# Optimization experiments

Hardware: AMD Instinct MI355X
Metric: run time of the kernel (lower is better)

## Reference

```python
import jax, jax.numpy as jnp
import numpy as np

B, S, HID, HEADS = 1, 512, 1024, 16
HD = HID // HEADS          # 64
LN_EPS = 1e-5
EPS = 1e-8


def setup_inputs() -> dict:
    key = jax.random.key(0)
    ks = jax.random.split(key, 10)
    def w(k, fan_in, shape):
        return (jax.random.normal(k, shape, jnp.float32) / np.sqrt(fan_in)).astype(jnp.float32)
    return {
        "x": jax.random.normal(ks[0], (B, S, HID), jnp.float32),
        "attention_mask": jnp.ones((B, S), jnp.int32),
        "Wq": w(ks[1], HID, (HID, HID)), "bq": jnp.zeros((HID,), jnp.float32),
        "Wk": w(ks[2], HID, (HID, HID)), "bk": jnp.zeros((HID,), jnp.float32),
        "Wv": w(ks[3], HID, (HID, HID)), "bv": jnp.zeros((HID,), jnp.float32),
        "Wo": w(ks[4], HID, (HID, HID)), "bo": jnp.zeros((HID,), jnp.float32),
        "temperature": jnp.ones((1,), jnp.float32),
        "ln_gamma": jnp.ones((HID,), jnp.float32),
        "ln_beta": jnp.zeros((HID,), jnp.float32),
    }


def _forward(x, attention_mask, Wq, bq, Wk, bk, Wv, bv, Wo, bo, temperature, ln_gamma, ln_beta):
    b, s, hid = x.shape
    residual = x
    def proj(W, bias):  # [b,s,hid] -> [b,H,s,hd]
        return (x @ W + bias).reshape(b, s, HEADS, HD).transpose(0, 2, 1, 3)
    Q, K, V = proj(Wq, bq), proj(Wk, bk), proj(Wv, bv)
    # FFT over head_dim -> F = HD//2+1 frequency bins
    Qf = jnp.fft.rfft(Q, axis=-1)
    Kf = jnp.fft.rfft(K, axis=-1)
    Qa, Ka = jnp.abs(Qf), jnp.abs(Kf)
    Qp, Kp = jnp.angle(Qf), jnp.angle(Kf)
    # broadcast to [b,H,Sq,Sk,F]; eps lives inside sqrt (faithful, non-factorized)
    amp_w = jnp.sqrt(Qa[:, :, :, None, :] * Ka[:, :, None, :, :] + EPS)
    phase_align = jnp.cos(Qp[:, :, :, None, :] - Kp[:, :, None, :, :])
    scores = jnp.sum(phase_align * amp_w, axis=-1) * temperature  # [b,H,Sq,Sk]
    mask = attention_mask[:, None, None, :]  # [b,1,1,Sk]
    scores = jnp.where(mask == 0, jnp.float32(-1e9), scores)
    attn = jax.nn.softmax(scores, axis=-1)   # dropout omitted (eval mode)
    out = jnp.einsum('bhqk,bhkd->bhqd', attn, V)
    out = out.transpose(0, 2, 1, 3).reshape(b, s, hid)
    out = out @ Wo + bo
    y = residual + out
    mu = jnp.mean(y, axis=-1, keepdims=True)
    var = jnp.var(y, axis=-1, keepdims=True)
    return (y - mu) / jnp.sqrt(var + LN_EPS) * ln_gamma + ln_beta


def reference(x, attention_mask, Wq, bq, Wk, bk, Wv, bv, Wo, bo, temperature, ln_gamma, ln_beta):
    return _forward(x, attention_mask, Wq, bq, Wk, bk, Wv, bv, Wo, bo,
                    temperature, ln_gamma, ln_beta)
```

## Files before the change

### kernel.cpp

```cpp
#include <hip/hip_runtime.h>
#include <hip/hip_bf16.h>
#include <math.h>

constexpr int SEQ   = 512;
constexpr int HIDC  = 1024;
constexpr int NH    = 16;
constexpr int HDIM  = 64;
constexpr int NFREQ = 33;
constexpr int NFP   = 128;

typedef unsigned short u16;
typedef __bf16 bf16x8 __attribute__((ext_vector_type(8)));
typedef float  f32x4  __attribute__((ext_vector_type(4)));
typedef unsigned short u16x8 __attribute__((ext_vector_type(8)));

typedef __attribute__((address_space(3))) void       as3_void;
typedef __attribute__((address_space(1))) const void as1_void;

__device__ __forceinline__ void gload16(const u16* g, u16* l) {
    __builtin_amdgcn_global_load_lds((as1_void*)g, (as3_void*)l, 16, 0, 0);
}

__device__ __forceinline__ float ldin(const void* p, int i, int f32) {
    if (f32) return ((const float*)p)[i];
    return __bfloat162float(((const __hip_bfloat16*)p)[i]);
}

__device__ __forceinline__ u16 f2b(float f) {
    unsigned int u = __builtin_bit_cast(unsigned int, f);
    u += 0x7fffu + ((u >> 16) & 1u);
    return (u16)(u >> 16);
}
__device__ __forceinline__ float b2f(u16 b) {
    return __builtin_bit_cast(float, (unsigned int)b << 16);
}
__device__ __forceinline__ void split2(float f, u16& hi, u16& lo) {
    hi = f2b(f);
    lo = f2b(f - b2f(hi));
}

__device__ __forceinline__ int sniffF(const u16* wq) {
    const int lane = threadIdx.x & 63;
    const ushort4 a = *(const ushort4*)(wq + lane * 8);
    const ushort4 b = *(const ushort4*)(wq + lane * 8 + 4);
    int bad = 0;
    {
        const u16 vs[8] = {a.x, a.y, a.z, a.w, b.x, b.y, b.z, b.w};
        #pragma unroll
        for (int j = 0; j < 8; ++j)
            if (((vs[j] >> 7) & 0xFF) >= 134) bad++;
    }
    #pragma unroll
    for (int off = 32; off > 0; off >>= 1) bad += __shfl_xor(bad, off, 64);
    return (bad > 32) ? 1 : 0;
}

__global__ __launch_bounds__(256) void prep_kernel(
    const void* __restrict__ W0, const void* __restrict__ W1,
    const void* __restrict__ W2, const void* __restrict__ W3,
    u16* __restrict__ H0, u16* __restrict__ L0,
    u16* __restrict__ H1, u16* __restrict__ L1,
    u16* __restrict__ H2, u16* __restrict__ L2,
    u16* __restrict__ H3, u16* __restrict__ L3,
    const void* __restrict__ xsrc, u16* __restrict__ xhi, u16* __restrict__ xlo)
{
    const int F  = sniffF((const u16*)W0);
    const int mz = blockIdx.z;

    if (mz == 4) {
        const int blk = blockIdx.y * 16 + blockIdx.x;
        const int i0  = blk * 2048 + threadIdx.x * 8;
        #pragma unroll
        for (int g = 0; g < 2; ++g) {
            const int i = i0 + g * 4;
            float v[4];
            if (F) {
                const float4 f = *(const float4*)((const float*)xsrc + i);
                v[0] = f.x; v[1] = f.y; v[2] = f.z; v[3] = f.w;
            } else {
                #pragma unroll
                for (int j = 0; j < 4; ++j) v[j] = ldin(xsrc, i + j, 0);
            }
            ushort4 oh, ol;
            u16 h, l;
            split2(v[0], h, l); oh.x = h; ol.x = l;
            split2(v[1], h, l); oh.y = h; ol.y = l;
            split2(v[2], h, l); oh.z = h; ol.z = l;
            split2(v[3], h, l); oh.w = h; ol.w = l;
            *(ushort4*)&xhi[i] = oh;
            *(ushort4*)&xlo[i] = ol;
        }
        return;
    }

    __shared__ float t[64][65];
    const void* W = (mz == 0) ? W0 : (mz == 1) ? W1 : (mz == 2) ? W2 : W3;
    u16* H = (mz == 0) ? H0 : (mz == 1) ? H1 : (mz == 2) ? H2 : H3;
    u16* L = (mz == 0) ? L0 : (mz == 1) ? L1 : (mz == 2) ? L2 : L3;
    const int n0 = blockIdx.x * 64, k0 = blockIdx.y * 64;
    const int tid = threadIdx.x;

    #pragma unroll
    for (int i = 0; i < 4; ++i) {
        const int item = i * 256 + tid;
        const int r = item >> 4, c4 = (item & 15) * 4;
        if (F) {
            const float4 v = *(const float4*)((const float*)W + (k0 + r) * HIDC + n0 + c4);
            t[r][c4 + 0] = v.x; t[r][c4 + 1] = v.y; t[r][c4 + 2] = v.z; t[r][c4 + 3] = v.w;
        } else {
            #pragma unroll
            for (int j = 0; j < 4; ++j)
                t[r][c4 + j] = ldin(W, (k0 + r) * HIDC + n0 + c4 + j, 0);
        }
    }
    __syncthreads();
    #pragma unroll
    for (int i = 0; i < 4; ++i) {
        const int item = i * 256 + tid;
        const int r = item >> 4, c4 = (item & 15) * 4;
        ushort4 oh, ol;
        u16 h, l;
        split2(t[c4 + 0][r], h, l); oh.x = h; ol.x = l;
        split2(t[c4 + 1][r], h, l); oh.y = h; ol.y = l;
        split2(t[c4 + 2][r], h, l); oh.z = h; ol.z = l;
        split2(t[c4 + 3][r], h, l); oh.w = h; ol.w = l;
        *(ushort4*)&H[(n0 + r) * HIDC + k0 + c4] = oh;
        *(ushort4*)&L[(n0 + r) * HIDC + k0 + c4] = ol;
    }
}

template <int MODE, int MT>
__global__ __launch_bounds__(256) void mfma3_gemm_kernel(
    const u16* __restrict__ Ahi, const u16* __restrict__ Alo,
    const u16* __restrict__ B0h, const u16* __restrict__ B0l,
    const u16* __restrict__ B1h, const u16* __restrict__ B1l,
    const u16* __restrict__ B2h, const u16* __restrict__ B2l,
    const void* __restrict__ b0, const void* __restrict__ b1, const void* __restrict__ b2,
    const void* __restrict__ xres,
    u16* __restrict__ Qh, u16* __restrict__ Ql,
    u16* __restrict__ Kh, u16* __restrict__ Kl,
    u16* __restrict__ Vth, u16* __restrict__ Vtl,
    float* __restrict__ Yout,
    const void* __restrict__ wq_sniff)
{
    constexpr int NMI = MT / 16;
    constexpr int NAC = MT / 32;
    constexpr int ACH = MT * 64;
    constexpr int BUF = 2 * ACH + 16384;
    __shared__ __align__(16) u16 smem[2 * BUF];

    const int F    = sniffF((const u16*)wq_sniff);
    const int tid  = threadIdx.x;
    const int lane = tid & 63, wv = tid >> 6;
    const int m0 = blockIdx.y * MT;
    const int n0 = blockIdx.x * 128;

    const u16 *Bh, *Bl; const void* bias; int col0, mat = 0;
    if (MODE == 0) {
        mat  = n0 >> 10;
        col0 = n0 & 1023;
        Bh   = (mat == 0) ? B0h : (mat == 1) ? B1h : B2h;
        Bl   = (mat == 0) ? B0l : (mat == 1) ? B1l : B2l;
        bias = (mat == 0) ? b0  : (mat == 1) ? b1  : b2;
    } else {
        col0 = n0; Bh = B0h; Bl = B0l; bias = b0;
    }

    const int rsub = lane >> 3;
    const int gsw  = ((lane & 7) ^ rsub) * 8;
    const u16* pAh[2]; const u16* pAl[2];
    const u16* pBh[4]; const u16* pBl[4];
    int dA[2], dB[4];
    #pragma unroll
    for (int j = 0; j < NAC; ++j) {
        const int c = wv * NAC + j;
        pAh[j] = Ahi + (m0 + c * 8 + rsub) * HIDC + gsw;
        pAl[j] = Alo + (m0 + c * 8 + rsub) * HIDC + gsw;
        dA[j]  = c * 512;
    }
    #pragma unroll
    for (int j = 0; j < 4; ++j) {
        const int c = wv * 4 + j;
        pBh[j] = Bh + (col0 + c * 8 + rsub) * HIDC + gsw;
        pBl[j] = Bl + (col0 + c * 8 + rsub) * HIDC + gsw;
        dB[j]  = c * 512;
    }

    int g16[2];
    #pragma unroll
    for (int kc = 0; kc < 2; ++kc) g16[kc] = (((kc * 4) + (lane >> 4)) ^ (lane & 7)) * 8;
    int afo[4], bfo[2];
    #pragma unroll
    for (int mi = 0; mi < NMI; ++mi) afo[mi] = (mi * 16 + (lane & 15)) * 64;
    #pragma unroll
    for (int ni = 0; ni < 2; ++ni) bfo[ni] = (wv * 32 + ni * 16 + (lane & 15)) * 64;

    f32x4 acc[NMI][2];
    #pragma unroll
    for (int mi = 0; mi < NMI; ++mi)
        #pragma unroll
        for (int ni = 0; ni < 2; ++ni) acc[mi][ni] = f32x4{0.f, 0.f, 0.f, 0.f};

    #pragma unroll
    for (int j = 0; j < NAC; ++j) {
        gload16(pAh[j], smem + dA[j]);
        gload16(pAl[j], smem + ACH + dA[j]);
    }
    #pragma unroll
    for (int j = 0; j < 4; ++j) {
        gload16(pBh[j], smem + 2 * ACH + dB[j]);
        gload16(pBl[j], smem + 2 * ACH + 8192 + dB[j]);
    }
    __syncthreads();

    for (int t = 0; t < 16; ++t) {
        const int bo = (t & 1) * BUF;
        if (t < 15) {
            const int bn = BUF - bo;
            const int k  = (t + 1) * 64;
            #pragma unroll
            for (int j = 0; j < NAC; ++j) {
                gload16(pAh[j] + k, smem + bn + dA[j]);
                gload16(pAl[j] + k, smem + bn + ACH + dA[j]);
            }
            #pragma unroll
            for (int j = 0; j < 4; ++j) {
                gload16(pBh[j] + k, smem + bn + 2 * ACH + dB[j]);
                gload16(pBl[j] + k, smem + bn + 2 * ACH + 8192 + dB[j]);
            }
        }
        #pragma unroll
        for (int kc = 0; kc < 2; ++kc) {
            bf16x8 ah[NMI], al[NMI], bh2[2], bl2[2];
            #pragma unroll
            for (int mi = 0; mi < NMI; ++mi) {
                ah[mi] = *(const bf16x8*)(smem + bo +       afo[mi] + g16[kc]);
                al[mi] = *(const bf16x8*)(smem + bo + ACH + afo[mi] + g16[kc]);
            }
            #pragma unroll
            for (int ni = 0; ni < 2; ++ni) {
                bh2[ni] = *(const bf16x8*)(smem + bo + 2 * ACH +        bfo[ni] + g16[kc]);
                bl2[ni] = *(const bf16x8*)(smem + bo + 2 * ACH + 8192 + bfo[ni] + g16[kc]);
            }
            #pragma unroll
            for (int mi = 0; mi < NMI; ++mi)
                #pragma unroll
                for (int ni = 0; ni < 2; ++ni) {
                    acc[mi][ni] = __builtin_amdgcn_mfma_f32_16x16x32_bf16(
                        ah[mi], bh2[ni], acc[mi][ni], 0, 0, 0);
                    acc[mi][ni] = __builtin_amdgcn_mfma_f32_16x16x32_bf16(
                        ah[mi], bl2[ni], acc[mi][ni], 0, 0, 0);
                    acc[mi][ni] = __builtin_amdgcn_mfma_f32_16x16x32_bf16(
                        al[mi], bh2[ni], acc[mi][ni], 0, 0, 0);
                }
        }
        __syncthreads();
    }

    const int hi4 = (lane >> 4) * 4;
    #pragma unroll
    for (int ni = 0; ni < 2; ++ni) {
        const int col = col0 + wv * 32 + ni * 16 + (lane & 15);
        const float bval = ldin(bias, col, F);
        #pragma unroll
        for (int mi = 0; mi < NMI; ++mi) {
            const int row0 = m0 + mi * 16 + hi4;
            if (MODE == 1) {
                #pragma unroll
                for (int r = 0; r < 4; ++r) {
                    const int row = row0 + r;
                    Yout[row * HIDC + col] =
                        acc[mi][ni][r] + bval + ldin(xres, row * HIDC + col, F);
                }
            } else if (mat == 2) {
                ushort4 oh, ol;
                u16 h_, l_;
                split2(acc[mi][ni][0] + bval, h_, l_); oh.x = h_; ol.x = l_;
                split2(acc[mi][ni][1] + bval, h_, l_); oh.y = h_; ol.y = l_;
                split2(acc[mi][ni][2] + bval, h_, l_); oh.z = h_; ol.z = l_;
                split2(acc[mi][ni][3] + bval, h_, l_); oh.w = h_; ol.w = l_;
                *(ushort4*)&Vth[col * SEQ + row0] = oh;
                *(ushort4*)&Vtl[col * SEQ + row0] = ol;
            } else {
                u16* Oh = (mat == 0) ? Qh : Kh;
                u16* Ol = (mat == 0) ? Ql : Kl;
                #pragma unroll
                for (int r = 0; r < 4; ++r) {
                    u16 h_, l_;
                    split2(acc[mi][ni][r] + bval, h_, l_);
                    Oh[(row0 + r) * HIDC + col] = h_;
                    Ol[(row0 + r) * HIDC + col] = l_;
                }
            }
        }
    }
}

__global__ __launch_bounds__(256) void dft_kernel(
    const u16* __restrict__ Qmh, const u16* __restrict__ Qml,
    const u16* __restrict__ Kmh, const u16* __restrict__ Kml,
    u16* __restrict__ Qsh, u16* __restrict__ Qsl,
    u16* __restrict__ Ksh, u16* __restrict__ Ksl)
{
    __shared__ __align__(16) u16 smem[16384];
    __shared__ float tcos[64], tsin[64];

    const int tid  = threadIdx.x;
    const int lane = tid & 63, wv = tid >> 6;
    const int hi = lane >> 4, q15 = lane & 15, l7 = lane & 7;
    const int m0  = blockIdx.x * 64;
    const int sel = blockIdx.y;
    const u16* Ah_g = sel ? Kmh : Qmh;
    const u16* Al_g = sel ? Kml : Qml;
    u16* Oh = sel ? Ksh : Qsh;
    u16* Ol = sel ? Ksl : Qsl;

    const int rsub = lane >> 3;
    const int gsw  = ((lane & 7) ^ rsub) * 8;
    #pragma unroll
    for (int j = 0; j < 2; ++j) {
        const int c = wv * 2 + j;
        gload16(Ah_g + (m0 + c * 8 + rsub) * 64 + gsw, smem + c * 512);
        gload16(Al_g + (m0 + c * 8 + rsub) * 64 + gsw, smem + 4096 + c * 512);
    }
    if (tid < 64) {
        float sv, cv;
        sincosf((float)tid * (6.283185307179586f / 64.0f), &sv, &cv);
        tcos[tid] = cv; tsin[tid] = sv;
    }
    __syncthreads();

    bf16x8 Dh[2][2], Dl[2][2];
    #pragma unroll
    for (int ni = 0; ni < 2; ++ni) {
        const int c = wv * 32 + ni * 16 + q15;
        #pragma unroll
        for (int kc = 0; kc < 2; ++kc) {
            u16x8 bh_, bl_;
            #pragma unroll
            for (int e = 0; e < 8; ++e) {
                const int k = (kc * 4 + hi) * 8 + e;
                float dv;
                if (c < 33)      dv = tcos[(c * k) & 63];
                else if (c < 66) dv = -tsin[((c - 33) * k) & 63];
                else             dv = 0.0f;
                u16 h_, l_;
                split2(dv, h_, l_);
                bh_[e] = h_; bl_[e] = l_;
            }
            Dh[ni][kc] = __builtin_bit_cast(bf16x8, bh_);
            Dl[ni][kc] = __builtin_bit_cast(bf16x8, bl_);
        }
    }

    f32x4 acc[4][2];
    #pragma unroll
    for (int mi = 0; mi < 4; ++mi)
        #pragma unroll
        for (int ni = 0; ni < 2; ++ni) acc[mi][ni] = f32x4{0.f, 0.f, 0.f, 0.f};

    #pragma unroll
    for (int kc = 0; kc < 2; ++kc) {
        const int g = (((kc * 4) + hi) ^ l7) * 8;
        bf16x8 ah[4], al[4];
        #pragma unroll
        for (int mi = 0; mi < 4; ++mi) {
            ah[mi] = *(const bf16x8*)(smem +        (mi * 16 + q15) * 64 + g);
            al[mi] = *(const bf16x8*)(smem + 4096 + (mi * 16 + q15) * 64 + g);
        }
        #pragma unroll
        for (int mi = 0; mi < 4; ++mi)
            #pragma unroll
            for (int ni = 0; ni < 2; ++ni) {
                acc[mi][ni] = __builtin_amdgcn_mfma_f32_16x16x32_bf16(
                    ah[mi], Dh[ni][kc], acc[mi][ni], 0, 0, 0);
                acc[mi][ni] = __builtin_amdgcn_mfma_f32_16x16x32_bf16(
                    ah[mi], Dl[ni][kc], acc[mi][ni], 0, 0, 0);
                acc[mi][ni] = __builtin_amdgcn_mfma_f32_16x16x32_bf16(
                    al[mi], Dh[ni][kc], acc[mi][ni], 0, 0, 0);
            }
    }
    __syncthreads();

    float* Cl = (float*)smem;
    #pragma unroll
    for (int mi = 0; mi < 4; ++mi)
        #pragma unroll
        for (int ni = 0; ni < 2; ++ni)
            #pragma unroll
            for (int r = 0; r < 4; ++r)
                Cl[(mi * 16 + hi * 4 + r) * 128 + wv * 32 + ni * 16 + q15] = acc[mi][ni][r];
    __syncthreads();

    const int row = tid >> 2, tf = tid & 3;
    const int g   = m0 + row;
    const int ss  = g >> 4, hh = g & 15;
    u16 vh[32], vl[32];
    #pragma unroll
    for (int j = 0; j < 32; ++j) {
        const int f = tf * 32 + j;
        float val = 0.0f;
        if (f < 66) {
            const int fb = (f < 33) ? f : (f - 33);
            const float re = Cl[row * 128 + fb];
            const float im = Cl[row * 128 + 33 + fb];
            const float a  = sqrtf(re * re + im * im);
            const float sc = (a > 0.0f) ? rsqrtf(a) : 0.0f;
            val = ((f < 33) ? re : im) * sc;
        }
        split2(val, vh[j], vl[j]);
    }
    const int obase = (hh * SEQ + ss) * NFP + tf * 32;
    #pragma unroll
    for (int j4 = 0; j4 < 8; ++j4) {
        ushort4 oh, ol;
        oh.x = vh[j4 * 4 + 0]; oh.y = vh[j4 * 4 + 1]; oh.z = vh[j4 * 4 + 2]; oh.w = vh[j4 * 4 + 3];
        ol.x = vl[j4 * 4 + 0]; ol.y = vl[j4 * 4 + 1]; ol.z = vl[j4 * 4 + 2]; ol.w = vl[j4 * 4 + 3];
        *(ushort4*)&Oh[obase + j4 * 4] = oh;
        *(ushort4*)&Ol[obase + j4 * 4] = ol;
    }
}

__global__ __launch_bounds__(128) void attn_mfma_kernel(
    const u16* __restrict__ Qsh, const u16* __restrict__ Qsl,
    const u16* __restrict__ Ksh, const u16* __restrict__ Ksl,
    const u16* __restrict__ VTh, const u16* __restrict__ VTl,
    const int* __restrict__ mask, const void* __restrict__ temp_p,
    u16* __restrict__ chi, u16* __restrict__ clo,
    const void* __restrict__ wq_sniff)
{
    __shared__ __align__(16) u16 smem[32768];
    __shared__ int   mask_lds[512];
    __shared__ float mpart[2][16], lpart[2][16], l_final[16];

    const int F    = sniffF((const u16*)wq_sniff);
    const int tid  = threadIdx.x;
    const int lane = tid & 63, w = tid >> 6;
    const int hi = lane >> 4, q15 = lane & 15, l7 = lane & 7;
    const int h  = blockIdx.y, q0 = blockIdx.x * 16;
    const int k0 = w * 256;
    const int WB = w * 16384;
    const float temp = ldin(temp_p, 0, F);

    *(int4*)&mask_lds[tid * 4] = *(const int4*)&mask[tid * 4];

    bf16x8 qfh[3], qfl[3];
    {
        const int qrow = (h * SEQ + q0 + q15) * NFP;
        #pragma unroll
        for (int kc = 0; kc < 3; ++kc) {
            qfh[kc] = *(const bf16x8*)(Qsh + qrow + kc * 32 + hi * 8);
            qfl[kc] = *(const bf16x8*)(Qsl + qrow + kc * 32 + hi * 8);
        }
    }

    const int rc4 = lane >> 4;

    auto stageK = [&](int kt, int b) {
        const int base = WB + b * 8192;
        #pragma unroll
        for (int j = 0; j < 8; ++j) {
            const int row = j * 4 + rc4;
            const int gs  = (q15 ^ (row & 7)) * 8;
            const int so  = (h * SEQ + k0 + kt * 32 + row) * NFP + gs;
            gload16(Ksh + so, smem + base + j * 512);
            gload16(Ksl + so, smem + base + 4096 + j * 512);
        }
    };
    auto stageV = [&](int c, int b) {
        const int base = WB + b * 4096;
        #pragma unroll
        for (int j = 0; j < 4; ++j) {
            const int d  = j * 16 + (lane >> 2);
            const int gs = ((lane & 3) ^ (d & 3)) * 8;
            const int so = (h * HDIM + d) * SEQ + k0 + c * 32 + gs;
            gload16(VTh + so, smem + base + j * 512);
            gload16(VTl + so, smem + base + 2048 + j * 512);
        }
    };

    f32x4 sT[16];
    #pragma unroll
    for (int t = 0; t < 16; ++t) sT[t] = f32x4{0.f, 0.f, 0.f, 0.f};

    stageK(0, 0);
    #pragma unroll
    for (int kt = 0; kt < 8; ++kt) {
        if (kt < 7) {
            stageK(kt + 1, (kt + 1) & 1);
            asm volatile("s_waitcnt vmcnt(16)" ::: "memory");
        } else {
            asm volatile("s_waitcnt vmcnt(0)" ::: "memory");
        }
        __builtin_amdgcn_sched_barrier(0);
        const int base = WB + (kt & 1) * 8192;
        #pragma unroll
        for (int tt = 0; tt < 2; ++tt) {
            #pragma unroll
            for (int kc = 0; kc < 3; ++kc) {
                const int ro = (tt * 16 + q15) * 128 + (((kc * 4 + hi) ^ l7) * 8);
                const bf16x8 ah = *(const bf16x8*)(smem + base + ro);
                const bf16x8 al = *(const bf16x8*)(smem + base + 4096 + ro);
                sT[kt * 2 + tt] = __builtin_amdgcn_mfma_f32_16x16x32_bf16(ah, qfh[kc], sT[kt * 2 + tt], 0, 0, 0);
                sT[kt * 2 + tt] = __builtin_amdgcn_mfma_f32_16x16x32_bf16(ah, qfl[kc], sT[kt * 2 + tt], 0, 0, 0);
                sT[kt * 2 + tt] = __builtin_amdgcn_mfma_f32_16x16x32_bf16(al, qfh[kc], sT[kt * 2 + tt], 0, 0, 0);
            }
        }
    }

    __builtin_amdgcn_sched_barrier(0);
    stageV(0, 0);

    float m = -1e30f;
    #pragma unroll
    for (int t = 0; t < 16; ++t) {
        const int4 mv = *(const int4*)&mask_lds[k0 + t * 16 + hi * 4];
        float s;
        s = (mv.x == 0) ? -1e9f : sT[t][0] * temp; sT[t][0] = s; m = fmaxf(m, s);
        s = (mv.y == 0) ? -1e9f : sT[t][1] * temp; sT[t][1] = s; m = fmaxf(m, s);
        s = (mv.z == 0) ? -1e9f : sT[t][2] * temp; sT[t][2] = s; m = fmaxf(m, s);
        s = (mv.w == 0) ? -1e9f : sT[t][3] * temp; sT[t][3] = s; m = fmaxf(m, s);
    }
    m = fmaxf(m, __shfl_xor(m, 16, 64));
    m = fmaxf(m, __shfl_xor(m, 32, 64));
    if (lane < 16) mpart[w][q15] = m;
    __syncthreads();
    const float gm = fmaxf(mpart[0][q15], mpart[1][q15]);
    float sum = 0.0f;
    #pragma unroll
    for (int t = 0; t < 16; ++t) {
        #pragma unroll
        for (int r = 0; r < 4; ++r) {
            const float p = __expf(sT[t][r] - gm);
            sT[t][r] = p;
            sum += p;
        }
    }
    sum += __shfl_xor(sum, 16, 64);
    sum += __shfl_xor(sum, 32, 64);
    if (lane < 16) lpart[w][q15] = sum;
    __syncthreads();
    if (tid < 16) l_final[tid] = lpart[0][tid] + lpart[1][tid];

    const int PH = WB + 8192, PL = PH + 640;
    f32x4 acc[4];
    #pragma unroll
    for (int dt = 0; dt < 4; ++dt) acc[dt] = f32x4{0.f, 0.f, 0.f, 0.f};

    #pragma unroll
    for (int c = 0; c < 8; ++c) {
        if (c < 7) {
            stageV(c + 1, (c + 1) & 1);
            asm volatile("s_waitcnt vmcnt(8)" ::: "memory");
        } else {
            asm volatile("s_waitcnt vmcnt(0)" ::: "memory");
        }
        __builtin_amdgcn_sched_barrier(0);
        #pragma unroll
        for (int tt = 0; tt < 2; ++tt) {
            const int t = c * 2 + tt;
            ushort4 ph, pl;
            u16 hh, ll;
            split2(sT[t][0], hh, ll); ph.x = hh; pl.x = ll;
            split2(sT[t][1], hh, ll); ph.y = hh; pl.y = ll;
            split2(sT[t][2], hh, ll); ph.z = hh; pl.z = ll;
            split2(sT[t][3], hh, ll); ph.w = hh; pl.w = ll;
            const int g  = tt * 2 + (hi >> 1);
            const int po = q15 * 40 + ((g ^ (q15 & 3)) * 8) + (hi & 1) * 4;
            *(ushort4*)(smem + PH + po) = ph;
            *(ushort4*)(smem + PL + po) = pl;
        }
        const int vb  = WB + (c & 1) * 4096;
        const int pro = q15 * 40 + ((hi ^ (q15 & 3)) * 8);
        const bf16x8 pfh = *(const bf16x8*)(smem + PH + pro);
        const bf16x8 pfl = *(const bf16x8*)(smem + PL + pro);
        #pragma unroll
        for (int dt = 0; dt < 4; ++dt) {
            const int vo = (dt * 16 + q15) * 32 + ((hi ^ (q15 & 3)) * 8);
            const bf16x8 vfh = *(const bf16x8*)(smem + vb + vo);
            const bf16x8 vfl = *(const bf16x8*)(smem + vb + 2048 + vo);
            acc[dt] = __builtin_amdgcn_mfma_f32_16x16x32_bf16(pfh, vfh, acc[dt], 0, 0, 0);
            acc[dt] = __builtin_amdgcn_mfma_f32_16x16x32_bf16(pfl, vfh, acc[dt], 0, 0, 0);
            acc[dt] = __builtin_amdgcn_mfma_f32_16x16x32_bf16(pfh, vfl, acc[dt], 0, 0, 0);
        }
    }

    float* pacc = (float*)(smem + WB + 12288);
    #pragma unroll
    for (int dt = 0; dt < 4; ++dt)
        *(f32x4*)&pacc[(dt * 64 + lane) * 4] = acc[dt];
    __syncthreads();
    const float* pa0 = (const float*)(smem + 12288);
    const float* pa1 = (const float*)(smem + 16384 + 12288);
    #pragma unroll
    for (int dd = 0; dd < 2; ++dd) {
        const int dt = w * 2 + dd;
        #pragma unroll
        for (int r = 0; r < 4; ++r) {
            const int idx = (dt * 64 + lane) * 4 + r;
            const float v = (pa0[idx] + pa1[idx]) / l_final[hi * 4 + r];
            u16 hh, ll;
            split2(v, hh, ll);
            const int row = q0 + hi * 4 + r;
            const int col = h * HDIM + dt * 16 + q15;
            chi[row * HIDC + col] = hh;
            clo[row * HIDC + col] = ll;
        }
    }
}

__global__ __launch_bounds__(256) void ln_kernel(
    const float* __restrict__ Y, const void* __restrict__ gamma,
    const void* __restrict__ beta, void* __restrict__ out,
    const void* __restrict__ wq_sniff)
{
    const int F = sniffF((const u16*)wq_sniff);
    const int row = blockIdx.x, tid = threadIdx.x;
    float v[4];
    float s = 0.0f, s2 = 0.0f;
    #pragma unroll
    for (int j = 0; j < 4; ++j) {
        v[j] = Y[row * HIDC + tid + j * 256];
        s += v[j]; s2 += v[j] * v[j];
    }
    #pragma unroll
    for (int off = 32; off > 0; off >>= 1) {
        s  += __shfl_xor(s, off, 64);
        s2 += __shfl_xor(s2, off, 64);
    }
    __shared__ float wred[4][2];
    const int w = tid >> 6;
    if ((tid & 63) == 0) { wred[w][0] = s; wred[w][1] = s2; }
    __syncthreads();
    s  = wred[0][0] + wred[1][0] + wred[2][0] + wred[3][0];
    s2 = wred[0][1] + wred[1][1] + wred[2][1] + wred[3][1];
    const float mu   = s / (float)HIDC;
    const float var  = s2 / (float)HIDC - mu * mu;
    const float rstd = rsqrtf(var + 1e-5f);
    #pragma unroll
    for (int j = 0; j < 4; ++j) {
        const int c = tid + j * 256;
        const float g = ldin(gamma, c, F), b = ldin(beta, c, F);
        const float r = (v[j] - mu) * rstd * g + b;
        if (F) ((float*)out)[row * HIDC + c] = r;
        else   ((__hip_bfloat16*)out)[row * HIDC + c] = __float2bfloat16(r);
    }
}

extern "C" void kernel_launch(void* const* d_in, const int* in_sizes, int n_in,
                              void* d_out, int out_size, void* d_ws, size_t ws_size,
                              hipStream_t stream) {
    const void* x    = d_in[0];
    const int*  mask = (const int*)d_in[1];
    const void* Wq   = d_in[2];
    const void* bq   = d_in[3];
    const void* Wk   = d_in[4];
    const void* bk   = d_in[5];
    const void* Wv   = d_in[6];
    const void* bv   = d_in[7];
    const void* Wo   = d_in[8];
    const void* bo   = d_in[9];
    const void* temp = d_in[10];
    const void* gam  = d_in[11];
    const void* bet  = d_in[12];

    float* Y    = (float*)d_ws;
    u16*   xhi  = (u16*)(Y + SEQ * HIDC);
    u16*   xlo  = xhi + SEQ * HIDC;
    u16*   chi  = xlo + SEQ * HIDC;
    u16*   clo  = chi + SEQ * HIDC;
    u16*   Qmh  = clo + SEQ * HIDC;
    u16*   Qml  = Qmh + SEQ * HIDC;
    u16*   Kmh  = Qml + SEQ * HIDC;
    u16*   Kml  = Kmh + SEQ * HIDC;
    u16*   VTh  = Kml + SEQ * HIDC;
    u16*   VTl  = VTh + NH * HDIM * SEQ;
    u16*   Wqh  = VTl + NH * HDIM * SEQ;
    u16*   Wql  = Wqh + HIDC * HIDC;
    u16*   Wkh  = Wql + HIDC * HIDC;
    u16*   Wkl  = Wkh + HIDC * HIDC;
    u16*   Wvh  = Wkl + HIDC * HIDC;
    u16*   Wvl  = Wvh + HIDC * HIDC;
    u16*   Woh  = Wvl + HIDC * HIDC;
    u16*   Wol  = Woh + HIDC * HIDC;
    u16*   Qsh  = Wol + HIDC * HIDC;
    u16*   Qsl  = Qsh + NH * SEQ * NFP;
    u16*   Ksh  = Qsl + NH * SEQ * NFP;
    u16*   Ksl  = Ksh + NH * SEQ * NFP;

    prep_kernel<<<dim3(16, 16, 5), 256, 0, stream>>>(
        Wq, Wk, Wv, Wo, Wqh, Wql, Wkh, Wkl, Wvh, Wvl, Woh, Wol,
        x, xhi, xlo);

    mfma3_gemm_kernel<0, 64><<<dim3(24, 8), 256, 0, stream>>>(
        xhi, xlo, Wqh, Wql, Wkh, Wkl, Wvh, Wvl,
        bq, bk, bv, nullptr,
        Qmh, Qml, Kmh, Kml, VTh, VTl, nullptr, Wq);

    dft_kernel<<<dim3(128, 2), 256, 0, stream>>>(
        Qmh, Qml, Kmh, Kml, Qsh, Qsl, Ksh, Ksl);

    attn_mfma_kernel<<<dim3(SEQ / 16, NH), 128, 0, stream>>>(
        Qsh, Qsl, Ksh, Ksl, VTh, VTl, mask, temp, chi, clo, Wq);

    mfma3_gemm_kernel<1, 32><<<dim3(8, 16), 256, 0, stream>>>(
        chi, clo, Woh, Wol, nullptr, nullptr, nullptr, nullptr,
        bo, nullptr, nullptr, x,
        nullptr, nullptr, nullptr, nullptr, nullptr, nullptr, Y, Wq);

    ln_kernel<<<SEQ, 256, 0, stream>>>(Y, gam, bet, d_out, Wq);
}
```

Measured before the change: 161.6 us.

## Fuse head-dim DFT and amplitude normalization into QKV projection GEMM epilogue

The separate DFT kernel is removed. The QKV GEMM epilogue now stages each 64x128 output tile (two heads) in shared memory, runs the 64-point DFT with split-bf16 MFMAs per head, applies the amplitude normalization, and writes the spectral Q/K buffers directly. This drops one kernel launch and the round trip of the intermediate Q/K projections through global memory. In exchange the Q and K GEMM blocks carry a longer serial epilogue with extra syncs and LDS traffic, which may lengthen the critical path of that kernel.

```diff
diff --git a/kernel.cpp b/kernel.cpp
--- a/kernel.cpp
+++ b/kernel.cpp
@@ -137,8 +137,8 @@
     const u16* __restrict__ B2h, const u16* __restrict__ B2l,
     const void* __restrict__ b0, const void* __restrict__ b1, const void* __restrict__ b2,
     const void* __restrict__ xres,
-    u16* __restrict__ Qh, u16* __restrict__ Ql,
-    u16* __restrict__ Kh, u16* __restrict__ Kl,
+    u16* __restrict__ Qsh, u16* __restrict__ Qsl,
+    u16* __restrict__ Ksh, u16* __restrict__ Ksl,
     u16* __restrict__ Vth, u16* __restrict__ Vtl,
     float* __restrict__ Yout,
     const void* __restrict__ wq_sniff)
@@ -148,10 +148,13 @@
     constexpr int ACH = MT * 64;
     constexpr int BUF = 2 * ACH + 16384;
     __shared__ __align__(16) u16 smem[2 * BUF];
+    __shared__ float tcs[64], tsn[64];
 
     const int F    = sniffF((const u16*)wq_sniff);
     const int tid  = threadIdx.x;
     const int lane = tid & 63, wv = tid >> 6;
+    const int q15 = lane & 15, hi = lane >> 4, l7 = lane & 7;
+    const int hi4 = hi * 4;
     const int m0 = blockIdx.y * MT;
     const int n0 = blockIdx.x * 128;
 
@@ -188,12 +191,12 @@
 
     int g16[2];
     #pragma unroll
-    for (int kc = 0; kc < 2; ++kc) g16[kc] = (((kc * 4) + (lane >> 4)) ^ (lane & 7)) * 8;
+    for (int kc = 0; kc < 2; ++kc) g16[kc] = (((kc * 4) + hi) ^ l7) * 8;
     int afo[4], bfo[2];
     #pragma unroll
-    for (int mi = 0; mi < NMI; ++mi) afo[mi] = (mi * 16 + (lane & 15)) * 64;
-    #pragma unroll
-    for (int ni = 0; ni < 2; ++ni) bfo[ni] = (wv * 32 + ni * 16 + (lane & 15)) * 64;
+    for (int mi = 0; mi < NMI; ++mi) afo[mi] = (mi * 16 + q15) * 64;
+    #pragma unroll
+    for (int ni = 0; ni < 2; ++ni) bfo[ni] = (wv * 32 + ni * 16 + q15) * 64;
 
     f32x4 acc[NMI][2];
     #pragma unroll
@@ -257,22 +260,30 @@
         __syncthreads();
     }
 
-    const int hi4 = (lane >> 4) * 4;
-    #pragma unroll
-    for (int ni = 0; ni < 2; ++ni) {
-        const int col = col0 + wv * 32 + ni * 16 + (lane & 15);
-        const float bval = ldin(bias, col, F);
-        #pragma unroll
-        for (int mi = 0; mi < NMI; ++mi) {
-            const int row0 = m0 + mi * 16 + hi4;
-            if (MODE == 1) {
+    if (MODE == 1) {
+        #pragma unroll
+        for (int ni = 0; ni < 2; ++ni) {
+            const int col = col0 + wv * 32 + ni * 16 + q15;
+            const float bval = ldin(bias, col, F);
+            #pragma unroll
+            for (int mi = 0; mi < NMI; ++mi) {
+                const int row0 = m0 + mi * 16 + hi4;
                 #pragma unroll
                 for (int r = 0; r < 4; ++r) {
                     const int row = row0 + r;
                     Yout[row * HIDC + col] =
                         acc[mi][ni][r] + bval + ldin(xres, row * HIDC + col, F);
                 }
-            } else if (mat == 2) {
+            }
+        }
+    } else if (mat == 2) {
+        #pragma unroll
+        for (int ni = 0; ni < 2; ++ni) {
+            const int col = col0 + wv * 32 + ni * 16 + q15;
+            const float bval = ldin(bias, col, F);
+            #pragma unroll
+            for (int mi = 0; mi < NMI; ++mi) {
+                const int row0 = m0 + mi * 16 + hi4;
                 ushort4 oh, ol;
                 u16 h_, l_;
                 split2(acc[mi][ni][0] + bval, h_, l_); oh.x = h_; ol.x = l_;
@@ -281,143 +292,138 @@
                 split2(acc[mi][ni][3] + bval, h_, l_); oh.w = h_; ol.w = l_;
                 *(ushort4*)&Vth[col * SEQ + row0] = oh;
                 *(ushort4*)&Vtl[col * SEQ + row0] = ol;
-            } else {
-                u16* Oh = (mat == 0) ? Qh : Kh;
-                u16* Ol = (mat == 0) ? Ql : Kl;
-                #pragma unroll
-                for (int r = 0; r < 4; ++r) {
+            }
+        }
+    } else {
+        float* Cf = (float*)smem;
+        #pragma unroll
+        for (int ni = 0; ni < 2; ++ni) {
+            const int c = wv * 32 + ni * 16 + q15;
+            const float bval = ldin(bias, col0 + c, F);
+            #pragma unroll
+            for (int mi = 0; mi < NMI; ++mi)
+                #pragma unroll
+                for (int r = 0; r < 4; ++r)
+                    Cf[(mi * 16 + hi4 + r) * 128 + c] = acc[mi][ni][r] + bval;
+        }
+        if (tid < 64) {
+            float sv, cv;
+            sincosf((float)tid * (6.283185307179586f / 64.0f), &sv, &cv);
+            tcs[tid] = cv; tsn[tid] = sv;
+        }
+        __syncthreads();
+
+        bf16x8 Dh[2][2], Dl[2][2];
+        #pragma unroll
+        for (int ni = 0; ni < 2; ++ni) {
+            const int c = wv * 32 + ni * 16 + q15;
+            #pragma unroll
+            for (int kc = 0; kc < 2; ++kc) {
+                u16x8 bh_, bl_;
+                #pragma unroll
+                for (int e = 0; e < 8; ++e) {
+                    const int k = (kc * 4 + hi) * 8 + e;
+                    float dv;
+                    if (c < 33)      dv = tcs[(c * k) & 63];
+                    else if (c < 66) dv = -tsn[((c - 33) * k) & 63];
+                    else             dv = 0.0f;
                     u16 h_, l_;
-                    split2(acc[mi][ni][r] + bval, h_, l_);
-                    Oh[(row0 + r) * HIDC + col] = h_;
-                    Ol[(row0 + r) * HIDC + col] = l_;
+                    split2(dv, h_, l_);
+                    bh_[e] = h_; bl_[e] = l_;
                 }
-            }
-        }
-    }
-}
-
-__global__ __launch_bounds__(256) void dft_kernel(
-    const u16* __restrict__ Qmh, const u16* __restrict__ Qml,
-    const u16* __restrict__ Kmh, const u16* __restrict__ Kml,
-    u16* __restrict__ Qsh, u16* __restrict__ Qsl,
-    u16* __restrict__ Ksh, u16* __restrict__ Ksl)
-{
-    __shared__ __align__(16) u16 smem[16384];
-    __shared__ float tcos[64], tsin[64];
-
-    const int tid  = threadIdx.x;
-    const int lane = tid & 63, wv = tid >> 6;
-    const int hi = lane >> 4, q15 = lane & 15, l7 = lane & 7;
-    const int m0  = blockIdx.x * 64;
-    const int sel = blockIdx.y;
-    const u16* Ah_g = sel ? Kmh : Qmh;
-    const u16* Al_g = sel ? Kml : Qml;
-    u16* Oh = sel ? Ksh : Qsh;
-    u16* Ol = sel ? Ksl : Qsl;
-
-    const int rsub = lane >> 3;
-    const int gsw  = ((lane & 7) ^ rsub) * 8;
-    #pragma unroll
-    for (int j = 0; j < 2; ++j) {
-        const int c = wv * 2 + j;
-        gload16(Ah_g + (m0 + c * 8 + rsub) * 64 + gsw, smem + c * 512);
-        gload16(Al_g + (m0 + c * 8 + rsub) * 64 + gsw, smem + 4096 + c * 512);
-    }
-    if (tid < 64) {
-        float sv, cv;
-        sincosf((float)tid * (6.283185307179586f / 64.0f), &sv, &cv);
-        tcos[tid] = cv; tsin[tid] = sv;
-    }
-    __syncthreads();
-
-    bf16x8 Dh[2][2], Dl[2][2];
-    #pragma unroll
-    for (int ni = 0; ni < 2; ++ni) {
-        const int c = wv * 32 + ni * 16 + q15;
-        #pragma unroll
-        for (int kc = 0; kc < 2; ++kc) {
-            u16x8 bh_, bl_;
-            #pragma unroll
-            for (int e = 0; e < 8; ++e) {
-                const int k = (kc * 4 + hi) * 8 + e;
-                float dv;
-                if (c < 33)      dv = tcos[(c * k) & 63];
-                else if (c < 66) dv = -tsin[((c - 33) * k) & 63];
-                else             dv = 0.0f;
-                u16 h_, l_;
-                split2(dv, h_, l_);
-                bh_[e] = h_; bl_[e] = l_;
-            }
-            Dh[ni][kc] = __builtin_bit_cast(bf16x8, bh_);
-            Dl[ni][kc] = __builtin_bit_cast(bf16x8, bl_);
-        }
-    }
-
-    f32x4 acc[4][2];
-    #pragma unroll
-    for (int mi = 0; mi < 4; ++mi)
-        #pragma unroll
-        for (int ni = 0; ni < 2; ++ni) acc[mi][ni] = f32x4{0.f, 0.f, 0.f, 0.f};
-
-    #pragma unroll
-    for (int kc = 0; kc < 2; ++kc) {
-        const int g = (((kc * 4) + hi) ^ l7) * 8;
-        bf16x8 ah[4], al[4];
-        #pragma unroll
-        for (int mi = 0; mi < 4; ++mi) {
-            ah[mi] = *(const bf16x8*)(smem +        (mi * 16 + q15) * 64 + g);
-            al[mi] = *(const bf16x8*)(smem + 4096 + (mi * 16 + q15) * 64 + g);
-        }
-        #pragma unroll
-        for (int mi = 0; mi < 4; ++mi)
-            #pragma unroll
-            for (int ni = 0; ni < 2; ++ni) {
-                acc[mi][ni] = __builtin_amdgcn_mfma_f32_16x16x32_bf16(
-                    ah[mi], Dh[ni][kc], acc[mi][ni], 0, 0, 0);
-                acc[mi][ni] = __builtin_amdgcn_mfma_f32_16x16x32_bf16(
-                    ah[mi], Dl[ni][kc], acc[mi][ni], 0, 0, 0);
-                acc[mi][ni] = __builtin_amdgcn_mfma_f32_16x16x32_bf16(
-                    al[mi], Dh[ni][kc], acc[mi][ni], 0, 0, 0);
-            }
-    }
-    __syncthreads();
-
-    float* Cl = (float*)smem;
-    #pragma unroll
-    for (int mi = 0; mi < 4; ++mi)
-        #pragma unroll
-        for (int ni = 0; ni < 2; ++ni)
-            #pragma unroll
-            for (int r = 0; r < 4; ++r)
-                Cl[(mi * 16 + hi * 4 + r) * 128 + wv * 32 + ni * 16 + q15] = acc[mi][ni][r];
-    __syncthreads();
-
-    const int row = tid >> 2, tf = tid & 3;
-    const int g   = m0 + row;
-    const int ss  = g >> 4, hh = g & 15;
-    u16 vh[32], vl[32];
-    #pragma unroll
-    for (int j = 0; j < 32; ++j) {
-        const int f = tf * 32 + j;
-        float val = 0.0f;
-        if (f < 66) {
-            const int fb = (f < 33) ? f : (f - 33);
-            const float re = Cl[row * 128 + fb];
-            const float im = Cl[row * 128 + 33 + fb];
-            const float a  = sqrtf(re * re + im * im);
-            const float sc = (a > 0.0f) ? rsqrtf(a) : 0.0f;
-            val = ((f < 33) ? re : im) * sc;
-        }
-        split2(val, vh[j], vl[j]);
-    }
-    const int obase = (hh * SEQ + ss) * NFP + tf * 32;
-    #pragma unroll
-    for (int j4 = 0; j4 < 8; ++j4) {
-        ushort4 oh, ol;
-        oh.x = vh[j4 * 4 + 0]; oh.y = vh[j4 * 4 + 1]; oh.z = vh[j4 * 4 + 2]; oh.w = vh[j4 * 4 + 3];
-        ol.x = vl[j4 * 4 + 0]; ol.y = vl[j4 * 4 + 1]; ol.z = vl[j4 * 4 + 2]; ol.w = vl[j4 * 4 + 3];
-        *(ushort4*)&Oh[obase + j4 * 4] = oh;
-        *(ushort4*)&Ol[obase + j4 * 4] = ol;
+                Dh[ni][kc] = __builtin_bit_cast(bf16x8, bh_);
+                Dl[ni][kc] = __builtin_bit_cast(bf16x8, bl_);
+            }
+        }
+
+        u16* AH = smem + 16384;
+        u16* AL = smem + 20480;
+        float* C2 = (float*)(smem + 24576);
+        u16* Oh = (mat == 0) ? Qsh : Ksh;
+        u16* Ol = (mat == 0) ? Qsl : Ksl;
+
+        #pragma unroll
+        for (int head = 0; head < 2; ++head) {
+            const int hh = (col0 >> 6) + head;
+            {
+                const int row = tid >> 2;
+                const int d0  = (tid & 3) * 16;
+                const int rx  = row & 7;
+                #pragma unroll
+                for (int d = d0; d < d0 + 16; ++d) {
+                    const int src = (((d >> 3) ^ rx) * 8) + (d & 7);
+                    u16 h_, l_;
+                    split2(Cf[row * 128 + head * 64 + src], h_, l_);
+                    AH[row * 64 + d] = h_;
+                    AL[row * 64 + d] = l_;
+                }
+            }
+            __syncthreads();
+            f32x4 a2[4][2];
+            #pragma unroll
+            for (int mi = 0; mi < 4; ++mi)
+                #pragma unroll
+                for (int ni = 0; ni < 2; ++ni) a2[mi][ni] = f32x4{0.f, 0.f, 0.f, 0.f};
+            #pragma unroll
+            for (int kc = 0; kc < 2; ++kc) {
+                const int g = g16[kc];
+                bf16x8 ah2[4], al2[4];
+                #pragma unroll
+                for (int mi = 0; mi < 4; ++mi) {
+                    ah2[mi] = *(const bf16x8*)(AH + (mi * 16 + q15) * 64 + g);
+                    al2[mi] = *(const bf16x8*)(AL + (mi * 16 + q15) * 64 + g);
+                }
+                #pragma unroll
+                for (int mi = 0; mi < 4; ++mi)
+                    #pragma unroll
+                    for (int ni = 0; ni < 2; ++ni) {
+                        a2[mi][ni] = __builtin_amdgcn_mfma_f32_16x16x32_bf16(
+                            ah2[mi], Dh[ni][kc], a2[mi][ni], 0, 0, 0);
+                        a2[mi][ni] = __builtin_amdgcn_mfma_f32_16x16x32_bf16(
+                            ah2[mi], Dl[ni][kc], a2[mi][ni], 0, 0, 0);
+                        a2[mi][ni] = __builtin_amdgcn_mfma_f32_16x16x32_bf16(
+                            al2[mi], Dh[ni][kc], a2[mi][ni], 0, 0, 0);
+                    }
+            }
+            __syncthreads();
+            #pragma unroll
+            for (int mi = 0; mi < 4; ++mi)
+                #pragma unroll
+                for (int ni = 0; ni < 2; ++ni)
+                    #pragma unroll
+                    for (int r = 0; r < 4; ++r)
+                        C2[(mi * 16 + hi4 + r) * 128 + wv * 32 + ni * 16 + q15] = a2[mi][ni][r];
+            __syncthreads();
+            {
+                const int row = tid >> 2, tf = tid & 3;
+                u16 vh[32], vl[32];
+                #pragma unroll
+                for (int j = 0; j < 32; ++j) {
+                    const int f = tf * 32 + j;
+                    float val = 0.0f;
+                    if (f < 66) {
+                        const int fb = (f < 33) ? f : (f - 33);
+                        const float re = C2[row * 128 + fb];
+                        const float im = C2[row * 128 + 33 + fb];
+                        const float a  = sqrtf(re * re + im * im);
+                        const float sc = (a > 0.0f) ? rsqrtf(a) : 0.0f;
+                        val = ((f < 33) ? re : im) * sc;
+                    }
+                    split2(val, vh[j], vl[j]);
+                }
+                const int obase = (hh * SEQ + m0 + row) * NFP + tf * 32;
+                #pragma unroll
+                for (int j4 = 0; j4 < 8; ++j4) {
+                    ushort4 oh, ol;
+                    oh.x = vh[j4 * 4 + 0]; oh.y = vh[j4 * 4 + 1];
+                    oh.z = vh[j4 * 4 + 2]; oh.w = vh[j4 * 4 + 3];
+                    ol.x = vl[j4 * 4 + 0]; ol.y = vl[j4 * 4 + 1];
+                    ol.z = vl[j4 * 4 + 2]; ol.w = vl[j4 * 4 + 3];
+                    *(ushort4*)&Oh[obase + j4 * 4] = oh;
+                    *(ushort4*)&Ol[obase + j4 * 4] = ol;
+                }
+            }
+        }
     }
 }
 
@@ -669,11 +675,7 @@
     u16*   xlo  = xhi + SEQ * HIDC;
     u16*   chi  = xlo + SEQ * HIDC;
     u16*   clo  = chi + SEQ * HIDC;
-    u16*   Qmh  = clo + SEQ * HIDC;
-    u16*   Qml  = Qmh + SEQ * HIDC;
-    u16*   Kmh  = Qml + SEQ * HIDC;
-    u16*   Kml  = Kmh + SEQ * HIDC;
-    u16*   VTh  = Kml + SEQ * HIDC;
+    u16*   VTh  = clo + SEQ * HIDC;
     u16*   VTl  = VTh + NH * HDIM * SEQ;
     u16*   Wqh  = VTl + NH * HDIM * SEQ;
     u16*   Wql  = Wqh + HIDC * HIDC;
@@ -695,10 +697,7 @@
     mfma3_gemm_kernel<0, 64><<<dim3(24, 8), 256, 0, stream>>>(
         xhi, xlo, Wqh, Wql, Wkh, Wkl, Wvh, Wvl,
         bq, bk, bv, nullptr,
-        Qmh, Qml, Kmh, Kml, VTh, VTl, nullptr, Wq);
-
-    dft_kernel<<<dim3(128, 2), 256, 0, stream>>>(
-        Qmh, Qml, Kmh, Kml, Qsh, Qsl, Ksh, Ksl);
+        Qsh, Qsl, Ksh, Ksl, VTh, VTl, nullptr, Wq);
 
     attn_mfma_kernel<<<dim3(SEQ / 16, NH), 128, 0, stream>>>(
         Qsh, Qsl, Ksh, Ksl, VTh, VTl, mask, temp, chi, clo, Wq);
```

Measured after the change: 173.4 us. 7.3% more time.
